# Kernel tuning notes

Measured on AMD Instinct MI355X. Metric: run time of the kernel, lower is better.

Reference implementation:

```python
import jax, jax.numpy as jnp
import numpy as np

B = 64
IN_CH = 256
CH = 128
OUT_CH = 256
RES = 16
EMBED = 64
N_EMBED = 1024
N_PHYLO = 64          # n_phylo_channels; non-phylo = CH - N_PHYLO = 64
CODES = 16            # codes_per_phylolevel
LEVELS = 4            # n_phylolevels == n_levels_non_attribute
BETA = 0.25
FLAT_IN = N_PHYLO * RES * RES          # 16384
FLAT_Z = EMBED * CODES * LEVELS        # 4096


def setup_inputs() -> dict:
    key = jax.random.key(0)
    ks = jax.random.split(key, 16)
    s = 0.02
    return {
        "x": jax.random.normal(ks[0], (B, IN_CH, RES, RES), jnp.float32),
        "conv_in_w": jax.random.normal(ks[1], (IN_CH, CH), jnp.float32) * s,
        "conv_in_b": jnp.zeros((CH,), jnp.float32),
        "ln_p_g": jnp.ones((N_PHYLO, RES, RES), jnp.float32),
        "ln_p_b": jnp.zeros((N_PHYLO, RES, RES), jnp.float32),
        "W_in_p": jax.random.normal(ks[2], (FLAT_IN, FLAT_Z), jnp.float32) * s,
        "b_in_p": jnp.zeros((FLAT_Z,), jnp.float32),
        "ln_n_g": jnp.ones((CH - N_PHYLO, RES, RES), jnp.float32),
        "ln_n_b": jnp.zeros((CH - N_PHYLO, RES, RES), jnp.float32),
        "W_in_n": jax.random.normal(ks[3], (FLAT_IN, FLAT_Z), jnp.float32) * s,
        "b_in_n": jnp.zeros((FLAT_Z,), jnp.float32),
        "codebook": jax.random.uniform(ks[4], (N_EMBED, EMBED), jnp.float32, -1.0 / N_EMBED, 1.0 / N_EMBED),
        "W_out_p": jax.random.normal(ks[5], (FLAT_Z, FLAT_IN), jnp.float32) * s,
        "b_out_p": jnp.zeros((FLAT_IN,), jnp.float32),
        "W_out_n": jax.random.normal(ks[6], (FLAT_Z, FLAT_IN), jnp.float32) * s,
        "b_out_n": jnp.zeros((FLAT_IN,), jnp.float32),
        "conv_out_w": jax.random.normal(ks[7], (CH, OUT_CH), jnp.float32) * s,
        "conv_out_b": jnp.zeros((OUT_CH,), jnp.float32),
    }


def _layernorm(h, g, b, eps=1e-5):
    # normalize over (C,H,W) per sample, affine params shaped (C,H,W)
    m = jnp.mean(h, axis=(1, 2, 3), keepdims=True)
    v = jnp.var(h, axis=(1, 2, 3), keepdims=True)
    return (h - m) * jax.lax.rsqrt(v + eps) * g + b


def _quantize(z, codebook, beta=BETA):
    # z: (B, E, C, L) treated as (b, c, h, w) by taming VQ
    zp = jnp.transpose(z, (0, 2, 3, 1))                       # (B, C, L, E)
    zf = zp.reshape(-1, zp.shape[-1])                          # (B*C*L, E)
    d = (jnp.sum(zf * zf, axis=1, keepdims=True)
         - 2.0 * zf @ codebook.T
         + jnp.sum(codebook * codebook, axis=1)[None, :])      # (N_tok, n_embed)
    idx = jnp.argmin(d, axis=1)
    zq = codebook[idx].reshape(zp.shape)
    sg = jax.lax.stop_gradient
    loss = jnp.mean((sg(zq) - zp) ** 2) + beta * jnp.mean((zq - sg(zp)) ** 2)
    zq = zp + sg(zq - zp)                                      # straight-through
    return jnp.transpose(zq, (0, 3, 1, 2)), loss


def reference(x, conv_in_w, conv_in_b, ln_p_g, ln_p_b, W_in_p, b_in_p,
              ln_n_g, ln_n_b, W_in_n, b_in_n, codebook,
              W_out_p, b_out_p, W_out_n, b_out_n, conv_out_w, conv_out_b):
    # conv_in: 1x1 conv + SiLU
    h = jax.nn.silu(jnp.einsum('bchw,cd->bdhw', x, conv_in_w) + conv_in_b[None, :, None, None])
    h_phylo, h_img = h[:, :N_PHYLO], h[:, N_PHYLO:]

    # mlp_in (LayerNorm -> Flatten -> Linear -> Unflatten)
    z_p = (_layernorm(h_phylo, ln_p_g, ln_p_b).reshape(B, -1) @ W_in_p + b_in_p).reshape(B, EMBED, CODES, LEVELS)
    z_n = (_layernorm(h_img, ln_n_g, ln_n_b).reshape(B, -1) @ W_in_n + b_in_n).reshape(B, EMBED, CODES, LEVELS)

    zq_p, loss_p = _quantize(z_p, codebook)
    zq_n, loss_n = _quantize(z_n, codebook)
    quant_loss = loss_p + loss_n

    # mlp_out (Flatten -> Linear -> Unflatten)
    hout_p = (zq_p.reshape(B, -1) @ W_out_p + b_out_p).reshape(B, N_PHYLO, RES, RES)
    hout_n = (zq_n.reshape(B, -1) @ W_out_n + b_out_n).reshape(B, CH - N_PHYLO, RES, RES)
    h_ = jnp.concatenate([hout_p, hout_n], axis=1)

    # conv_out: SiLU -> 1x1 conv
    out = jnp.einsum('bchw,cd->bdhw', jax.nn.silu(h_), conv_out_w) + conv_out_b[None, :, None, None]
    return out, quant_loss
```

## Files before the change

### kernel.cpp

```cpp
#include <hip/hip_runtime.h>
#include <hip/hip_bf16.h>
#include <math.h>

#define BB 64
#define IN_CH 256
#define CH 128
#define OUT_CH 256
#define SP 256
#define EMBED 64
#define N_EMBED 1024
#define NPH 64
#define FLAT_IN 16384
#define FLAT_Z 4096

typedef short bf16x8 __attribute__((ext_vector_type(8)));
typedef float f32x4 __attribute__((ext_vector_type(4)));

__device__ __forceinline__ float silu_f(float x){ return x / (1.0f + expf(-x)); }

__device__ __forceinline__ void gl_lds16(const void* g, void* l){
  __builtin_amdgcn_global_load_lds(
      (const __attribute__((address_space(1))) void*)g,
      (__attribute__((address_space(3))) void*)l, 16, 0, 0);
}

__global__ __launch_bounds__(256) void k_fused_in(const float* __restrict__ x,
    const float* __restrict__ w1, const float* __restrict__ b1,
    const float* __restrict__ gp, const float* __restrict__ bp,
    const float* __restrict__ gn, const float* __restrict__ bnl,
    __hip_bfloat16* __restrict__ Ahi)
{
  int b = blockIdx.x, ws = blockIdx.y;
  int t = threadIdx.x;
  int d0 = ws*64;
  float acc[64];
  #pragma unroll
  for (int j=0;j<64;j++) acc[j] = b1[d0+j];
  const float* xb = x + (size_t)b*IN_CH*SP + t;
  for (int c=0;c<IN_CH;c++){
    float xv = xb[(size_t)c*SP];
    #pragma unroll
    for (int j=0;j<64;j++) acc[j] = fmaf(xv, w1[c*CH + d0 + j], acc[j]);
  }
  double s1=0.0, s2=0.0;
  #pragma unroll
  for (int j=0;j<64;j++){
    float v = silu_f(acc[j]);
    acc[j] = v;
    double dv = (double)v;
    s1 += dv; s2 += dv*dv;
  }
  __shared__ double l1[256], l2[256];
  l1[t]=s1; l2[t]=s2; __syncthreads();
  for (int s=128; s>0; s>>=1){
    if (t<s){ l1[t]+=l1[t+s]; l2[t]+=l2[t+s]; }
    __syncthreads();
  }
  double m = l1[0]/(double)FLAT_IN;
  double v = l2[0]/(double)FLAT_IN - m*m;
  float mf = (float)m;
  float rs = (float)(1.0/sqrt(v+1e-5));
  const float* g  = ws? gn : gp;
  const float* bb = ws? bnl: bp;
  __hip_bfloat16* oh = Ahi + ((size_t)ws*64 + b)*FLAT_IN;
  #pragma unroll 4
  for (int j=0;j<64;j++){
    int k = j*256 + t;
    float val = fmaf((acc[j]-mf)*rs, g[k], bb[k]);
    oh[k] = __float2bfloat16(val);
  }
}

template<int N, int K>
__global__ __launch_bounds__(256) void k_gemm_mfma(
    const __hip_bfloat16* __restrict__ A,
    const float* __restrict__ W0, const float* __restrict__ W1,
    float* __restrict__ part, int CHUNK, int KC)
{
  __shared__ float wlds[4*4096];
  __shared__ float alds[4*1024];
  int nt = blockIdx.x, kc = blockIdx.y, wsel = blockIdx.z;
  const float* W = wsel ? W1 : W0;
  int t = threadIdx.x;
  int wave = t >> 6, lane = t & 63;
  int rl = lane & 15;
  int g  = lane >> 4;
  int kg = g * 8;
  int nbase = nt*128;
  int k0 = kc*CHUNK;

  const __hip_bfloat16* Aw = A + (size_t)wsel*64*K;

  int s_lane = ((g&1)<<4) | ((g&2)<<1);
  int wbase0 = kg*128 + ((wave*32 + rl) ^ s_lane);
  int wbase1 = kg*128 + ((wave*32 + 16 + rl) ^ s_lane);
  int abyte[4];
  #pragma unroll
  for (int mf=0; mf<4; ++mf)
    abyte[mf] = (mf*16+rl)*64 + ((g ^ ((rl>>1)&3))<<4);

  int src_off[4]; int dst_base[4];
  #pragma unroll
  for (int i=0;i<4;i++){
    int fi = (i*4+wave)*256 + lane*4;
    int kl = fi>>7, nn = fi&127;
    int s = (((kl>>3)&1)<<4) | (((kl>>3)&2)<<1);
    src_off[i] = kl*N + nbase + (nn ^ s);
    dst_base[i] = (i*4+wave)*256;
  }
  size_t a_src = (size_t)(t>>2)*K + (size_t)(((t&3)^((t>>3)&3))*8);
  int a_dst = wave*256;

  f32x4 acc[4][2];
  #pragma unroll
  for (int mf=0; mf<4; ++mf){ acc[mf][0] = (f32x4){0,0,0,0}; acc[mf][1] = (f32x4){0,0,0,0}; }

  auto STAGE = [&](int buf, int ks){
    const float* Wr = W + (size_t)(k0 + ks*32)*N;
    float* lb = &wlds[buf*4096];
    #pragma unroll
    for (int i=0;i<4;i++) gl_lds16(Wr + src_off[i], lb + dst_base[i]);
    gl_lds16(Aw + a_src + (size_t)(k0 + ks*32), &alds[buf*1024] + a_dst);
  };

  int NT_ = CHUNK/32;
  STAGE(0, 0);
  STAGE(1, 1);
  STAGE(2, 2);

  for (int ks=0; ks<NT_; ++ks){
    int cur = ks & 3;
    __builtin_amdgcn_sched_barrier(0);
    if (ks < NT_-2)       { asm volatile("s_waitcnt vmcnt(10)" ::: "memory"); }
    else if (ks == NT_-2) { asm volatile("s_waitcnt vmcnt(5)"  ::: "memory"); }
    else                  { asm volatile("s_waitcnt vmcnt(0)"  ::: "memory"); }
    __builtin_amdgcn_sched_barrier(0);
    __builtin_amdgcn_s_barrier();
    __builtin_amdgcn_sched_barrier(0);
    if (ks+3 < NT_) STAGE((ks+3)&3, ks+3);
    __builtin_amdgcn_sched_barrier(0);

    const float* lb = &wlds[cur*4096];
    const char* ab = (const char*)&alds[cur*1024];
    bf16x8 ah[4];
    #pragma unroll
    for (int mf=0; mf<4; ++mf) ah[mf] = *(const bf16x8*)(ab + abyte[mf]);
    float wv0[8], wv1[8];
    #pragma unroll
    for (int j=0;j<8;j++){ wv0[j] = lb[wbase0 + j*128]; wv1[j] = lb[wbase1 + j*128]; }
    bf16x8 bh0, bh1;
    #pragma unroll
    for (int j=0;j<8;j++){
      bh0[j] = __builtin_bit_cast(short, __float2bfloat16(wv0[j]));
      bh1[j] = __builtin_bit_cast(short, __float2bfloat16(wv1[j]));
    }
    #pragma unroll
    for (int mf=0; mf<4; ++mf){
      acc[mf][0] = __builtin_amdgcn_mfma_f32_16x16x32_bf16(ah[mf], bh0, acc[mf][0], 0,0,0);
      acc[mf][1] = __builtin_amdgcn_mfma_f32_16x16x32_bf16(ah[mf], bh1, acc[mf][1], 0,0,0);
    }
  }

  float* P = part + ((size_t)((wsel*KC + kc)*64))*N + nbase + wave*32 + rl;
  #pragma unroll
  for (int mf=0; mf<4; ++mf)
    #pragma unroll
    for (int f=0; f<2; ++f)
      #pragma unroll
      for (int r=0; r<4; ++r)
        P[((size_t)(mf*16 + g*4 + r))*N + f*16] = acc[mf][f][r];
}

__global__ __launch_bounds__(256) void k_zreduce(const float* __restrict__ part,
  const float* __restrict__ bp, const float* __restrict__ bn,
  float* __restrict__ z, int KC)
{
  int idx = blockIdx.x*256 + threadIdx.x;
  int ws = idx >> 18; int rem = idx & 262143;
  int m = rem >> 12; int n = rem & 4095;
  float s = (ws? bn: bp)[n];
  const float* p = part + ((size_t)ws*KC*64 + m)*4096 + n;
  for (int kc=0;kc<KC;kc++) s += p[(size_t)kc*64*4096];
  z[idx] = s;
}

__global__ __launch_bounds__(256) void k_qscan(const float* __restrict__ z,
  const float* __restrict__ cb,
  float* __restrict__ bests, int* __restrict__ bestj)
{
  int cs = blockIdx.y;
  int j0 = cs*64;
  __shared__ float cc_l[64];
  if (threadIdx.x < 64){
    const float* c = cb + (size_t)(j0+threadIdx.x)*EMBED;
    float s=0.f;
    #pragma unroll
    for (int e=0;e<EMBED;e++){ float cv=c[e]; s = fmaf(cv,cv,s); }
    cc_l[threadIdx.x]=s;
  }
  __syncthreads();
  int r = blockIdx.x*256 + threadIdx.x;
  int ws = r>>12, rem = r&4095; int b = rem>>6, rr = rem&63;
  const float* zr = z + (size_t)ws*BB*FLAT_Z + (size_t)b*FLAT_Z + rr;
  float zr_[EMBED];
  #pragma unroll
  for (int e=0;e<EMBED;e++) zr_[e] = zr[(size_t)e*64];
  float best = 3.4e38f; int bj = 0;
  for (int jj=0;jj<64;jj++){
    int j = j0 + jj;
    const float* c = cb + (size_t)j*EMBED;
    float s1 = 0.f;
    #pragma unroll
    for (int e=0;e<EMBED;e++) s1 = fmaf(c[e], zr_[e], s1);
    float s = fmaf(-2.f, s1, cc_l[jj]);
    if (s < best){ best = s; bj = j; }
  }
  bests[(size_t)cs*8192 + r] = best;
  bestj[(size_t)cs*8192 + r] = bj;
}

__global__ __launch_bounds__(256) void k_qfin(const float* __restrict__ z,
  const float* __restrict__ cb, const float* __restrict__ bests, const int* __restrict__ bestj,
  __hip_bfloat16* __restrict__ zqA, float* __restrict__ row_sse)
{
  int r = blockIdx.x*256 + threadIdx.x;
  float best = 3.4e38f; int bj = 0;
  for (int cs=0;cs<16;cs++){
    float v = bests[(size_t)cs*8192 + r];
    int j = bestj[(size_t)cs*8192 + r];
    if (v < best){ best=v; bj=j; }
  }
  int ws = r>>12, rem = r&4095; int b = rem>>6, rr = rem&63;
  const float* zr = z + (size_t)ws*BB*FLAT_Z + (size_t)b*FLAT_Z + rr;
  const float* c = cb + (size_t)bj*EMBED;
  __hip_bfloat16* zq = zqA + ((size_t)ws*64 + b)*FLAT_Z;
  float sse = 0.f;
  #pragma unroll
  for (int e=0;e<EMBED;e++){
    float cv = c[e];
    float zv = zr[(size_t)e*64];
    float d = cv - zv; sse = fmaf(d,d,sse);
    zq[(size_t)e*64 + rr] = __float2bfloat16(cv);
  }
  row_sse[r] = sse;
}

__global__ __launch_bounds__(256) void k_loss(const float* __restrict__ row_sse, float* __restrict__ out){
  __shared__ double l[256];
  double s=0.0;
  for (int i=threadIdx.x;i<8192;i+=256) s += (double)row_sse[i];
  l[threadIdx.x]=s; __syncthreads();
  for (int st=128;st>0;st>>=1){ if (threadIdx.x<st) l[threadIdx.x]+=l[threadIdx.x+st]; __syncthreads(); }
  if (threadIdx.x==0) out[(size_t)BB*OUT_CH*SP] = (float)(l[0]*1.25/262144.0);
}

__global__ __launch_bounds__(256) void k_hreduce(const float* __restrict__ part,
  const float* __restrict__ bp, const float* __restrict__ bn,
  float* __restrict__ hbuf, int KC)
{
  int idx = blockIdx.x*256 + threadIdx.x;
  int ws = idx >> 20; int rem = idx & 1048575;
  int m = rem >> 14; int n = rem & 16383;
  float s = (ws? bn: bp)[n];
  const float* p = part + ((size_t)ws*KC*64 + m)*16384 + n;
  for (int kc=0;kc<KC;kc++) s += p[(size_t)kc*64*16384];
  hbuf[((size_t)m*CH + ws*NPH + (n>>8))*SP + (n&255)] = s;
}

__global__ __launch_bounds__(256) void k_conv_out(const float* __restrict__ hbuf,
  const float* __restrict__ w2, const float* __restrict__ b2, float* __restrict__ out)
{
  int b = blockIdx.x, dg = blockIdx.y;
  int p = threadIdx.x;
  int d0 = dg*64;
  float acc[64];
  #pragma unroll
  for (int j=0;j<64;j++) acc[j]=b2[d0+j];
  const float* hb = hbuf + (size_t)b*CH*SP + p;
  for (int c=0;c<CH;c++){
    float hv = silu_f(hb[(size_t)c*SP]);
    #pragma unroll
    for (int j=0;j<64;j++) acc[j] = fmaf(hv, w2[c*OUT_CH + d0 + j], acc[j]);
  }
  float* ob = out + (size_t)b*OUT_CH*SP + (size_t)d0*SP + p;
  #pragma unroll
  for (int j=0;j<64;j++) ob[(size_t)j*SP] = acc[j];
}

extern "C" void kernel_launch(void* const* d_in, const int* in_sizes, int n_in,
                              void* d_out, int out_size, void* d_ws, size_t ws_size,
                              hipStream_t stream)
{
  const float* x   = (const float*)d_in[0];
  const float* w1  = (const float*)d_in[1];
  const float* b1  = (const float*)d_in[2];
  const float* gp  = (const float*)d_in[3];
  const float* bp  = (const float*)d_in[4];
  const float* Wip = (const float*)d_in[5];
  const float* bip = (const float*)d_in[6];
  const float* gn  = (const float*)d_in[7];
  const float* bnl = (const float*)d_in[8];
  const float* Win = (const float*)d_in[9];
  const float* bin = (const float*)d_in[10];
  const float* cb  = (const float*)d_in[11];
  const float* Wop = (const float*)d_in[12];
  const float* bop = (const float*)d_in[13];
  const float* Won = (const float*)d_in[14];
  const float* bon = (const float*)d_in[15];
  const float* w2  = (const float*)d_in[16];
  const float* b2  = (const float*)d_in[17];
  float* out = (float*)d_out;
  float* ws  = (float*)d_ws;

  __hip_bfloat16* Ahi = (__hip_bfloat16*)ws;
  float* z    = ws + 1048576;
  __hip_bfloat16* zqA = (__hip_bfloat16*)(ws + 1572864);
  float* hh   = ws + 1835008;
  float* sse  = ws + 3933184;
  float* bests= ws + 3941376;
  int*   bestj= (int*)(ws + 4072448);
  float* part = ws + 4203520;

  size_t wsf = ws_size/4;
  int KCe=8, KCd=2;
  if (wsf < (size_t)4203520 + 4194304) { KCe=4; KCd=1; }

  k_fused_in<<<dim3(64,2),256,0,stream>>>(x,w1,b1,gp,bp,gn,bnl,Ahi);
  k_gemm_mfma<4096,16384><<<dim3(32,KCe,2),256,0,stream>>>(Ahi,Wip,Win,part,16384/KCe,KCe);
  k_zreduce<<<2048,256,0,stream>>>(part,bip,bin,z,KCe);
  k_qscan<<<dim3(32,16),256,0,stream>>>(z,cb,bests,bestj);
  k_qfin<<<32,256,0,stream>>>(z,cb,bests,bestj,zqA,sse);
  k_gemm_mfma<16384,4096><<<dim3(128,KCd,2),256,0,stream>>>(zqA,Wop,Won,part,4096/KCd,KCd);
  k_hreduce<<<8192,256,0,stream>>>(part,bop,bon,hh,KCd);
  k_conv_out<<<dim3(64,4),256,0,stream>>>(hh,w2,b2,out);
  k_loss<<<1,256,0,stream>>>(sse,out);
}
```

Before: 444.5 us.

## Replace direct-to-LDS loads with register-staged double buffering and raise split-K

The GEMM kernel drops the global_load_lds 4-stage LDS ring. It now loads W and A tiles into registers three steps ahead and writes them into a 2-buffer LDS ring, with the XOR swizzle applied on the LDS write side. It also adds a launch-bounds occupancy hint of 4 blocks and doubles the split-K factor for both GEMMs when workspace allows. The aim is more resident blocks and more parallelism over the large weight streams, at the cost of extra register pressure, an explicit LDS store per step, more partial-sum traffic, and heavier reduce kernels.

```diff
diff --git a/kernel.cpp b/kernel.cpp
--- a/kernel.cpp
+++ b/kernel.cpp
@@ -17,12 +17,6 @@
 typedef float f32x4 __attribute__((ext_vector_type(4)));
 
 __device__ __forceinline__ float silu_f(float x){ return x / (1.0f + expf(-x)); }
-
-__device__ __forceinline__ void gl_lds16(const void* g, void* l){
-  __builtin_amdgcn_global_load_lds(
-      (const __attribute__((address_space(1))) void*)g,
-      (__attribute__((address_space(3))) void*)l, 16, 0, 0);
-}
 
 __global__ __launch_bounds__(256) void k_fused_in(const float* __restrict__ x,
     const float* __restrict__ w1, const float* __restrict__ b1,
@@ -72,13 +66,13 @@
 }
 
 template<int N, int K>
-__global__ __launch_bounds__(256) void k_gemm_mfma(
+__global__ __launch_bounds__(256,4) void k_gemm_mfma(
     const __hip_bfloat16* __restrict__ A,
     const float* __restrict__ W0, const float* __restrict__ W1,
     float* __restrict__ part, int CHUNK, int KC)
 {
-  __shared__ float wlds[4*4096];
-  __shared__ float alds[4*1024];
+  __shared__ float wlds[2*4096];
+  __shared__ float alds[2*1024];
   int nt = blockIdx.x, kc = blockIdx.y, wsel = blockIdx.z;
   const float* W = wsel ? W1 : W0;
   int t = threadIdx.x;
@@ -99,66 +93,87 @@
   for (int mf=0; mf<4; ++mf)
     abyte[mf] = (mf*16+rl)*64 + ((g ^ ((rl>>1)&3))<<4);
 
-  int src_off[4]; int dst_base[4];
+  int wsrc[4], wdst[4];
   #pragma unroll
   for (int i=0;i<4;i++){
-    int fi = (i*4+wave)*256 + lane*4;
-    int kl = fi>>7, nn = fi&127;
+    int kl = (i*4+wave)*2 + (lane>>5);
+    int nn = (lane&31)*4;
     int s = (((kl>>3)&1)<<4) | (((kl>>3)&2)<<1);
-    src_off[i] = kl*N + nbase + (nn ^ s);
-    dst_base[i] = (i*4+wave)*256;
-  }
-  size_t a_src = (size_t)(t>>2)*K + (size_t)(((t&3)^((t>>3)&3))*8);
-  int a_dst = wave*256;
+    wsrc[i] = kl*N + nbase + nn;
+    wdst[i] = kl*128 + (nn ^ s);
+  }
+  const f32x4* asrc = (const f32x4*)(Aw + (size_t)(t>>2)*K + (size_t)(t&3)*8 + k0);
+  int adst_b = (t>>2)*64 + (((t&3)^((t>>3)&3))<<4);
 
   f32x4 acc[4][2];
   #pragma unroll
   for (int mf=0; mf<4; ++mf){ acc[mf][0] = (f32x4){0,0,0,0}; acc[mf][1] = (f32x4){0,0,0,0}; }
 
-  auto STAGE = [&](int buf, int ks){
-    const float* Wr = W + (size_t)(k0 + ks*32)*N;
-    float* lb = &wlds[buf*4096];
-    #pragma unroll
-    for (int i=0;i<4;i++) gl_lds16(Wr + src_off[i], lb + dst_base[i]);
-    gl_lds16(Aw + a_src + (size_t)(k0 + ks*32), &alds[buf*1024] + a_dst);
-  };
+  float4 wA[4], aA, wB[4], aB;
 
   int NT_ = CHUNK/32;
-  STAGE(0, 0);
-  STAGE(1, 1);
-  STAGE(2, 2);
-
-  for (int ks=0; ks<NT_; ++ks){
-    int cur = ks & 3;
-    __builtin_amdgcn_sched_barrier(0);
-    if (ks < NT_-2)       { asm volatile("s_waitcnt vmcnt(10)" ::: "memory"); }
-    else if (ks == NT_-2) { asm volatile("s_waitcnt vmcnt(5)"  ::: "memory"); }
-    else                  { asm volatile("s_waitcnt vmcnt(0)"  ::: "memory"); }
-    __builtin_amdgcn_sched_barrier(0);
-    __builtin_amdgcn_s_barrier();
-    __builtin_amdgcn_sched_barrier(0);
-    if (ks+3 < NT_) STAGE((ks+3)&3, ks+3);
-    __builtin_amdgcn_sched_barrier(0);
-
-    const float* lb = &wlds[cur*4096];
-    const char* ab = (const char*)&alds[cur*1024];
-    bf16x8 ah[4];
-    #pragma unroll
-    for (int mf=0; mf<4; ++mf) ah[mf] = *(const bf16x8*)(ab + abyte[mf]);
-    float wv0[8], wv1[8];
-    #pragma unroll
-    for (int j=0;j<8;j++){ wv0[j] = lb[wbase0 + j*128]; wv1[j] = lb[wbase1 + j*128]; }
-    bf16x8 bh0, bh1;
-    #pragma unroll
-    for (int j=0;j<8;j++){
-      bh0[j] = __builtin_bit_cast(short, __float2bfloat16(wv0[j]));
-      bh1[j] = __builtin_bit_cast(short, __float2bfloat16(wv1[j]));
-    }
-    #pragma unroll
-    for (int mf=0; mf<4; ++mf){
-      acc[mf][0] = __builtin_amdgcn_mfma_f32_16x16x32_bf16(ah[mf], bh0, acc[mf][0], 0,0,0);
-      acc[mf][1] = __builtin_amdgcn_mfma_f32_16x16x32_bf16(ah[mf], bh1, acc[mf][1], 0,0,0);
-    }
+
+#define LOADSET(WREG, AREG, KS) { \
+    const float* Wr = W + (size_t)(k0 + (KS)*32)*N; \
+    _Pragma("unroll") \
+    for (int i=0;i<4;i++) WREG[i] = *(const float4*)(Wr + wsrc[i]); \
+    AREG = *(const float4*)(asrc + (size_t)(KS)*4); }
+
+#define WRITESET(WREG, AREG, BUF) { \
+    float* lb = &wlds[(BUF)*4096]; \
+    _Pragma("unroll") \
+    for (int i=0;i<4;i++) *(float4*)(lb + wdst[i]) = WREG[i]; \
+    *(float4*)((char*)&alds[(BUF)*1024] + adst_b) = AREG; }
+
+#define COMPUTE(BUF) { \
+    const float* lb = &wlds[(BUF)*4096]; \
+    const char* ab = (const char*)&alds[(BUF)*1024]; \
+    bf16x8 ah[4]; \
+    _Pragma("unroll") \
+    for (int mf=0; mf<4; ++mf) ah[mf] = *(const bf16x8*)(ab + abyte[mf]); \
+    float wv0[8], wv1[8]; \
+    _Pragma("unroll") \
+    for (int j=0;j<8;j++){ wv0[j] = lb[wbase0 + j*128]; wv1[j] = lb[wbase1 + j*128]; } \
+    bf16x8 bh0, bh1; \
+    _Pragma("unroll") \
+    for (int j=0;j<8;j++){ \
+      bh0[j] = __builtin_bit_cast(short, __float2bfloat16(wv0[j])); \
+      bh1[j] = __builtin_bit_cast(short, __float2bfloat16(wv1[j])); } \
+    _Pragma("unroll") \
+    for (int mf=0; mf<4; ++mf){ \
+      acc[mf][0] = __builtin_amdgcn_mfma_f32_16x16x32_bf16(ah[mf], bh0, acc[mf][0], 0,0,0); \
+      acc[mf][1] = __builtin_amdgcn_mfma_f32_16x16x32_bf16(ah[mf], bh1, acc[mf][1], 0,0,0); } }
+
+#define STEP(KS, WREG, AREG, WRBUF, RDBUF) { \
+    if ((KS)+1 < NT_) { \
+      if ((KS)+2 < NT_) { asm volatile("s_waitcnt vmcnt(5)" ::: "memory"); } \
+      else              { asm volatile("s_waitcnt vmcnt(0)" ::: "memory"); } \
+      __builtin_amdgcn_sched_barrier(0); \
+      WRITESET(WREG, AREG, WRBUF); \
+      if ((KS)+3 < NT_) LOADSET(WREG, AREG, (KS)+3); \
+    } \
+    asm volatile("s_waitcnt lgkmcnt(0)" ::: "memory"); \
+    __builtin_amdgcn_sched_barrier(0); \
+    __builtin_amdgcn_s_barrier(); \
+    __builtin_amdgcn_sched_barrier(0); \
+    COMPUTE(RDBUF); \
+    __builtin_amdgcn_sched_barrier(0); \
+    __builtin_amdgcn_s_barrier(); }
+
+  LOADSET(wA, aA, 0);
+  LOADSET(wB, aB, 1);
+  asm volatile("s_waitcnt vmcnt(5)" ::: "memory");
+  __builtin_amdgcn_sched_barrier(0);
+  WRITESET(wA, aA, 0);
+  if (2 < NT_) LOADSET(wA, aA, 2);
+  asm volatile("s_waitcnt lgkmcnt(0)" ::: "memory");
+  __builtin_amdgcn_sched_barrier(0);
+  __builtin_amdgcn_s_barrier();
+  __builtin_amdgcn_sched_barrier(0);
+
+  for (int k=0; k<NT_; k+=2){
+    STEP(k,   wB, aB, 1, 0);
+    STEP(k+1, wA, aA, 0, 1);
   }
 
   float* P = part + ((size_t)((wsel*KC + kc)*64))*N + nbase + wave*32 + rl;
@@ -169,6 +184,10 @@
       #pragma unroll
       for (int r=0; r<4; ++r)
         P[((size_t)(mf*16 + g*4 + r))*N + f*16] = acc[mf][f][r];
+#undef LOADSET
+#undef WRITESET
+#undef COMPUTE
+#undef STEP
 }
 
 __global__ __launch_bounds__(256) void k_zreduce(const float* __restrict__ part,
@@ -322,8 +341,9 @@
   float* part = ws + 4203520;
 
   size_t wsf = ws_size/4;
-  int KCe=8, KCd=2;
-  if (wsf < (size_t)4203520 + 4194304) { KCe=4; KCd=1; }
+  int KCe=16, KCd=4;
+  if (wsf < (size_t)4203520 + 8388608) { KCe=8;  KCd=2; }
+  if (wsf < (size_t)4203520 + 4194304) { KCe=4;  KCd=1; }
 
   k_fused_in<<<dim3(64,2),256,0,stream>>>(x,w1,b1,gp,bp,gn,bnl,Ahi);
   k_gemm_mfma<4096,16384><<<dim3(32,KCe,2),256,0,stream>>>(Ahi,Wip,Win,part,16384/KCe,KCe);
```

Measured after the change: 723.8 us. 1.63x slower.
